# Kernel optimization log

Hardware: AMD Instinct MI355X
Metric: run time of the kernel (lower is better)

The kernel has to match this reference:

```python
import jax, jax.numpy as jnp
import numpy as np

EPS_LN = 1e-6
EPS_NORM = 1e-7


def conv1x1(x, w, b):
    # x: [B,Cin,H,W], w: [Cout,Cin], b: [Cout]
    return jnp.einsum('bchw,oc->bohw', x, w) + b[None, :, None, None]


def ln2d(x, g, beta):
    u = x.mean(1, keepdims=True)
    s = ((x - u) ** 2).mean(1, keepdims=True)
    return g[None, :, None, None] * ((x - u) / jnp.sqrt(s + EPS_LN)) + beta[None, :, None, None]


def gather_neighborhoods(x, r):
    # x: [B,C,H,W] -> [B,C,n,H,W] with zero padding, n=(2r+1)**2
    B, C, H, W = x.shape
    xp = jnp.pad(x, ((0, 0), (0, 0), (r, r), (r, r)))
    slices = [xp[:, :, dy:dy + H, dx:dx + W]
              for dy in range(2 * r + 1) for dx in range(2 * r + 1)]
    return jnp.stack(slices, axis=2)


def valid_mask(H, W, r):
    offs = jnp.arange(-r, r + 1)
    hh = jnp.arange(H)
    ww = jnp.arange(W)
    vy = ((hh[None, :] + offs[:, None]) >= 0) & ((hh[None, :] + offs[:, None]) < H)  # [d,H]
    vx = ((ww[None, :] + offs[:, None]) >= 0) & ((ww[None, :] + offs[:, None]) < W)  # [d,W]
    return (vy[:, None, :, None] & vx[None, :, None, :]).reshape((2 * r + 1) ** 2, H, W)


def setup_inputs() -> dict:
    key = jax.random.key(0)
    B, C, H, W, r = 2, 64, 112, 112, 3
    n2 = (2 * r + 1) ** 2  # 49
    ks = jax.random.split(key, 16)
    s = 0.02
    inp = {
        'spatial_feats': jax.random.normal(ks[0], (B, C, H, W), jnp.float32),
        'semantic_feats': jax.random.normal(ks[1], (B, C, H, W), jnp.float32),
        # range_proj: conv1x1 -> LN2d -> SiLU -> conv1x1
        'rp_w1': s * jax.random.normal(ks[2], (C, C), jnp.float32), 'rp_b1': jnp.zeros((C,), jnp.float32),
        'rp_g': jnp.ones((C,), jnp.float32), 'rp_beta': jnp.zeros((C,), jnp.float32),
        'rp_w2': s * jax.random.normal(ks[3], (C, C), jnp.float32), 'rp_b2': jnp.zeros((C,), jnp.float32),
        # fixup_proj: conv1x1 (n2+C -> n2) -> LN2d -> SiLU -> conv1x1 (n2->n2)
        'fx_w1': s * jax.random.normal(ks[4], (n2, n2 + C), jnp.float32), 'fx_b1': jnp.zeros((n2,), jnp.float32),
        'fx_g': jnp.ones((n2,), jnp.float32), 'fx_beta': jnp.zeros((n2,), jnp.float32),
        'fx_w2': s * jax.random.normal(ks[5], (n2, n2), jnp.float32), 'fx_b2': jnp.zeros((n2,), jnp.float32),
        # output_proj: conv1x1 -> LN2d -> conv1x1
        'op_w1': s * jax.random.normal(ks[6], (C, C), jnp.float32), 'op_b1': jnp.zeros((C,), jnp.float32),
        'op_g': jnp.ones((C,), jnp.float32), 'op_beta': jnp.zeros((C,), jnp.float32),
        'op_w2': s * jax.random.normal(ks[7], (C, C), jnp.float32), 'op_b2': jnp.zeros((C,), jnp.float32),
        'sigma_spatial': jnp.array(1.0, jnp.float32),
    }
    return inp


def reference(spatial_feats, semantic_feats,
              rp_w1, rp_b1, rp_g, rp_beta, rp_w2, rp_b2,
              fx_w1, fx_b1, fx_g, fx_beta, fx_w2, fx_b2,
              op_w1, op_b1, op_g, op_beta, op_w2, op_b2,
              sigma_spatial):
    r = 3
    B, C, H, W = spatial_feats.shape
    # range_proj(semantic)
    px = conv1x1(semantic_feats, rp_w1, rp_b1)
    px = jax.nn.silu(ln2d(px, rp_g, rp_beta))
    px = conv1x1(px, rp_w2, rp_b2)

    # bilateral combined kernel: spatial Gaussian * range Gaussian, zero outside bounds
    offs = jnp.arange(-r, r + 1, dtype=jnp.float32)
    d2 = (offs[:, None] ** 2 + offs[None, :] ** 2).reshape(-1)  # [n2]
    sw = jnp.exp(-d2 / (2.0 * sigma_spatial ** 2))              # [n2]

    nbr = gather_neighborhoods(px, r)                            # [B,C,n2,H,W]
    nbr_sq = (nbr ** 2).sum(1)                                   # [B,n2,H,W]
    ctr_sq = (px ** 2).sum(1)                                    # [B,H,W]
    dot = jnp.einsum('bcnhw,bchw->bnhw', nbr, px)
    dist2 = jnp.maximum(nbr_sq + ctr_sq[:, None] - 2.0 * dot, 0.0)
    rw = jnp.exp(-dist2 / (2.0 * C))                             # range Gaussian, scale^2 = dim

    valid = valid_mask(H, W, r).astype(px.dtype)                 # [n2,H,W]
    combined = rw * sw[None, :, None, None] * valid[None]        # [B,n2,H,W]

    # gated fixup
    f = conv1x1(jnp.concatenate([combined, semantic_feats], axis=1), fx_w1, fx_b1)
    f = jax.nn.silu(ln2d(f, fx_g, fx_beta))
    f = conv1x1(f, fx_w2, fx_b2)
    combined = combined * (1.0 + jax.nn.sigmoid(f))
    combined = combined / (combined.sum(1, keepdims=True) + EPS_NORM)

    # neighborhood-weighted reduction of spatial feats
    nbhd = gather_neighborhoods(spatial_feats, r)                # [B,C,n2,H,W]
    out = jnp.einsum('bcnhw,bnhw->bchw', nbhd, combined)

    out = conv1x1(out, op_w1, op_b1)
    out = ln2d(out, op_g, op_beta)
    out = conv1x1(out, op_w2, op_b2)
    return out
```

## Files before the change

kernel.cpp:

```cpp
#include <hip/hip_runtime.h>

typedef unsigned short ushort;
typedef unsigned int uint;

constexpr int B = 2, C = 64, H = 112, W = 112;
constexpr int HW = H * W;
constexpr int NPIX = B * HW;
constexpr int NBLK = 512;
constexpr float EPS_LN = 1e-6f, EPS_NORM = 1e-7f;

typedef __attribute__((ext_vector_type(8))) short bf16x8;
typedef __attribute__((ext_vector_type(4))) float f32x4;

__device__ __forceinline__ float rcp_fast(float x) { return __builtin_amdgcn_rcpf(x); }
__device__ __forceinline__ float sigmoid_f(float x) { return rcp_fast(1.f + __expf(-x)); }
__device__ __forceinline__ int uni(int x) { return __builtin_amdgcn_readfirstlane(x); }
__device__ __forceinline__ int div7s(int x)  { return (x * 9363) >> 16; }
__device__ __forceinline__ int div13s(int x) { return (x * 5042) >> 16; }
__device__ __forceinline__ int div49s(int x) { return (x * 1338) >> 16; }

__device__ __forceinline__ ushort rne16(float x) {
    uint u = __float_as_uint(x);
    u += 0x7fffu + ((u >> 16) & 1u);
    return (ushort)(u >> 16);
}
__device__ __forceinline__ uint pack2(float a, float b) {
    return (uint)rne16(a) | ((uint)rne16(b) << 16);
}
__device__ __forceinline__ float2 up2(uint u) {
    return make_float2(__uint_as_float(u << 16), __uint_as_float(u & 0xffff0000u));
}

__device__ __forceinline__ f32x4 mfma16(bf16x8 a, bf16x8 b, f32x4 c) {
    return __builtin_amdgcn_mfma_f32_16x16x32_bf16(a, b, c, 0, 0, 0);
}

__device__ __forceinline__ void decode_blk(int blk, int& b, int& ty, int& tx) {
    int p8 = blk & 7, i = blk >> 3;
    b = p8 >> 2;
    int quad = p8 & 3;
    int lty = i >> 3, ltx = i & 7;
    ty = (quad >> 1) * 8 + lty;
    tx = (quad & 1) * 8 + ltx;
}

__device__ __forceinline__ void stage_w(const float* __restrict__ wsrc,
                                        ushort* wh, ushort* wl, int tid)
{
#pragma unroll
    for (int i = 0; i < 8; ++i) {
        int idx2 = i * 256 + tid;
        int o = idx2 >> 5, k = (idx2 & 31) * 2;
        float2 xy = *(const float2*)&wsrc[o * 64 + k];
        uint h = pack2(xy.x, xy.y);
        *(uint*)&wh[o * 72 + k] = h;
        *(uint*)&wl[o * 72 + k] = pack2(xy.x - __uint_as_float((h & 0xffffu) << 16),
                                        xy.y - __uint_as_float(h & 0xffff0000u));
    }
}

__device__ __forceinline__ void gemm64(const ushort* __restrict__ wh, const ushort* __restrict__ wl,
                                       const ushort* __restrict__ xh, const ushort* __restrict__ xl,
                                       const float* __restrict__ bias,
                                       int lm, int l4, int pp, f32x4 acc[4])
{
#pragma unroll
    for (int mt = 0; mt < 4; ++mt) {
        const int ob = mt * 16 + l4 * 4;
        acc[mt][0] = bias[ob]; acc[mt][1] = bias[ob + 1];
        acc[mt][2] = bias[ob + 2]; acc[mt][3] = bias[ob + 3];
    }
#pragma unroll
    for (int kt = 0; kt < 2; ++kt) {
        const int xo = pp * 72 + kt * 32 + l4 * 8;
        bf16x8 bh = *(const bf16x8*)&xh[xo];
        bf16x8 bl = *(const bf16x8*)&xl[xo];
#pragma unroll
        for (int mt = 0; mt < 4; ++mt) {
            const int wo = (mt * 16 + lm) * 72 + kt * 32 + l4 * 8;
            bf16x8 ah = *(const bf16x8*)&wh[wo];
            bf16x8 al = *(const bf16x8*)&wl[wo];
            acc[mt] = mfma16(al, bh, acc[mt]);
            acc[mt] = mfma16(ah, bl, acc[mt]);
            acc[mt] = mfma16(ah, bh, acc[mt]);
        }
    }
}

__global__ __launch_bounds__(256) void k1_range_proj(
    const float* __restrict__ sem,
    const float* __restrict__ w1, const float* __restrict__ b1,
    const float* __restrict__ g,  const float* __restrict__ be,
    const float* __restrict__ w2, const float* __restrict__ b2,
    ushort* __restrict__ px16, float* __restrict__ sqnorm)
{
    __shared__ __align__(16) ushort u16[28160];
    ushort* wh1 = u16;
    ushort* wl1 = u16 + 4608;
    ushort* wh2 = u16 + 9216;
    ushort* wl2 = u16 + 13824;
    ushort* xh  = u16 + 18432;
    ushort* xl  = u16 + 23040;
    float*  bv  = (float*)(u16 + 27648);

    const int tid = threadIdx.x, lane = tid & 63, wv = tid >> 6;
    const int lm = lane & 15, l4 = lane >> 4;
    int b, ty, tx; decode_blk(blockIdx.x, b, ty, tx);

    {
        const int lp = lane < 49 ? lane : 48;
        const int py = div7s(lp), px = lp - py * 7;
        const int hw = (ty * 7 + py) * W + tx * 7 + px;
        const bool a = lane < 49;
        float xv[16];
#pragma unroll
        for (int j = 0; j < 16; ++j)
            xv[j] = a ? sem[(size_t)(b * 64 + wv * 16 + j) * HW + hw] : 0.f;
        uint hu[8], lu[8];
#pragma unroll
        for (int jj = 0; jj < 8; ++jj) {
            uint hh = pack2(xv[2 * jj], xv[2 * jj + 1]);
            hu[jj] = hh;
            lu[jj] = pack2(xv[2 * jj]     - __uint_as_float((hh & 0xffffu) << 16),
                           xv[2 * jj + 1] - __uint_as_float(hh & 0xffff0000u));
        }
        const int rb = lane * 72 + wv * 16;
        *(uint4*)&xh[rb]     = make_uint4(hu[0], hu[1], hu[2], hu[3]);
        *(uint4*)&xh[rb + 8] = make_uint4(hu[4], hu[5], hu[6], hu[7]);
        *(uint4*)&xl[rb]     = make_uint4(lu[0], lu[1], lu[2], lu[3]);
        *(uint4*)&xl[rb + 8] = make_uint4(lu[4], lu[5], lu[6], lu[7]);
    }
    stage_w(w1, wh1, wl1, tid);
    stage_w(w2, wh2, wl2, tid);
    if (tid < 64) { bv[tid] = b1[tid]; bv[64 + tid] = g[tid];
                    bv[128 + tid] = be[tid]; bv[192 + tid] = b2[tid]; }
    __syncthreads();

    const int pp = wv * 16 + lm;
    f32x4 f[4];
    gemm64(wh1, wl1, xh, xl, bv, lm, l4, pp, f);

    float psum = 0.f, psq = 0.f;
#pragma unroll
    for (int mt = 0; mt < 4; ++mt)
#pragma unroll
        for (int r = 0; r < 4; ++r) { float fv = f[mt][r]; psum += fv; psq += fv * fv; }
    psum += __shfl_xor(psum, 16); psum += __shfl_xor(psum, 32);
    psq  += __shfl_xor(psq, 16);  psq  += __shfl_xor(psq, 32);
    const float m = psum * (1.f / 64.f);
    const float rstd = rsqrtf(psq * (1.f / 64.f) - m * m + EPS_LN);

    float sv_[16];
#pragma unroll
    for (int mt = 0; mt < 4; ++mt)
#pragma unroll
        for (int r = 0; r < 4; ++r) {
            const int o = mt * 16 + l4 * 4 + r;
            float y = bv[64 + o] * (f[mt][r] - m) * rstd + bv[128 + o];
            sv_[mt * 4 + r] = y * sigmoid_f(y);
        }
    __syncthreads();
#pragma unroll
    for (int mt = 0; mt < 4; ++mt) {
        uint h0 = pack2(sv_[4 * mt],     sv_[4 * mt + 1]);
        uint h1 = pack2(sv_[4 * mt + 2], sv_[4 * mt + 3]);
        uint l0 = pack2(sv_[4 * mt]     - __uint_as_float((h0 & 0xffffu) << 16),
                        sv_[4 * mt + 1] - __uint_as_float(h0 & 0xffff0000u));
        uint l1 = pack2(sv_[4 * mt + 2] - __uint_as_float((h1 & 0xffffu) << 16),
                        sv_[4 * mt + 3] - __uint_as_float(h1 & 0xffff0000u));
        const int so = pp * 72 + mt * 16 + l4 * 4;
        *(uint2*)&xh[so] = make_uint2(h0, h1);
        *(uint2*)&xl[so] = make_uint2(l0, l1);
    }
    __syncthreads();

    f32x4 z[4];
    gemm64(wh2, wl2, xh, xl, bv + 192, lm, l4, pp, z);

    float sq = 0.f;
#pragma unroll
    for (int mt = 0; mt < 4; ++mt)
#pragma unroll
        for (int r = 0; r < 4; ++r) sq += z[mt][r] * z[mt][r];
    sq += __shfl_xor(sq, 16); sq += __shfl_xor(sq, 32);

    if (pp < 49) {
        const int py = div7s(pp), px = pp - py * 7;
        const int hwi = (ty * 7 + py) * W + tx * 7 + px;
        ushort* dst = &px16[((size_t)b * HW + hwi) * 64];
#pragma unroll
        for (int mt = 0; mt < 4; ++mt)
            *(uint2*)&dst[mt * 16 + l4 * 4] =
                make_uint2(pack2(z[mt][0], z[mt][1]), pack2(z[mt][2], z[mt][3]));
        if (l4 == 0) sqnorm[(size_t)b * HW + hwi] = sq;
    }
}

__global__ __launch_bounds__(256, 2) void k23_fused(
    const ushort* __restrict__ px16, const float* __restrict__ sqnorm,
    const float* __restrict__ sem,  const float* __restrict__ spat,
    const float* __restrict__ fw1, const float* __restrict__ fb1,
    const float* __restrict__ fg,  const float* __restrict__ fbe,
    const float* __restrict__ fw2, const float* __restrict__ fb2,
    const float* __restrict__ w1, const float* __restrict__ b1,
    const float* __restrict__ g,  const float* __restrict__ be,
    const float* __restrict__ w2, const float* __restrict__ b2,
    const float* __restrict__ sigma_, float* __restrict__ out)
{
    __shared__ __align__(16) float smem[18048];
    ushort* haloA = (ushort*)smem;
    ushort* haloB = (ushort*)(smem + 5408);
    float*  comb  = smem + 10816;
    float*  fscr  = smem + 13952;
    float*  sqn_l = smem + 17088;
    float*  pm3   = smem + 17264;
    float*  ps3   = smem + 17520;
    float*  pt    = smem + 17776;
    float*  fwc  = smem;
    float*  fw2l = smem + 2401;
    ushort* whiP = (ushort*)smem;
    ushort* wloP = (ushort*)smem + 4608;
    ushort* ahiP = (ushort*)(smem + 5408);
    ushort* aloP = (ushort*)(smem + 5408) + 4608;
    float*  bvP  = smem + 13952;

    const int tid = threadIdx.x, lane = tid & 63, wv = tid >> 6;
    const int lm = lane & 15, l4 = lane >> 6 == 0 ? (lane >> 4) : 0;
    int b, ty, tx; decode_blk(blockIdx.x, b, ty, tx);
    const int lp  = lane < 49 ? lane : 48;
    const int py  = div7s(lp), pxl = lp - py * 7;
    const int h = ty * 7 + py, w = tx * 7 + pxl;
    const int hw = h * W + w;
    const int h0 = ty * 7 - 3, w0 = tx * 7 - 3;
    const bool act = lane < 49;

    float sv[64];
#pragma unroll
    for (int k = 0; k < 64; ++k) sv[k] = sem[(size_t)(b * 64 + k) * HW + hw];

    if (tid < 169) {
        const int ry = div13s(tid), rx = tid - ry * 13;
        const int hh = h0 + ry, ww = w0 + rx;
        const bool valid = (unsigned)hh < (unsigned)H && (unsigned)ww < (unsigned)W;
        const int soff = hh * W + ww;
        const int rsw = (tid & 7), rb_ = tid << 6;
#pragma unroll
        for (int cq = 0; cq < 8; ++cq) {
            uint4 v = make_uint4(0u, 0u, 0u, 0u);
            if (valid) {
                const float* sp = &spat[(size_t)(b * 64 + 8 * cq) * HW + soff];
                v.x = pack2(sp[0],      sp[HW]);
                v.y = pack2(sp[2 * HW], sp[3 * HW]);
                v.z = pack2(sp[4 * HW], sp[5 * HW]);
                v.w = pack2(sp[6 * HW], sp[7 * HW]);
            }
            *(uint4*)&haloB[rb_ + ((cq ^ rsw) << 3)] = v;
        }
    }

    for (int i = 0; i < 6; ++i) {
        int idx = i * 256 + tid;
        if (idx < 1352) {
            int r = idx >> 3, q = idx & 7;
            int ry = div13s(r), rx = r - ry * 13;
            int hh = h0 + ry, ww = w0 + rx;
            bool valid = (unsigned)hh < (unsigned)H && (unsigned)ww < (unsigned)W;
            uint4 v = make_uint4(0u, 0u, 0u, 0u);
            if (valid) v = *(const uint4*)&px16[((size_t)b * HW + hh * W + ww) * 64 + 8 * q];
            *(uint4*)&haloA[(r << 6) + ((q ^ (r & 7)) << 3)] = v;
        }
    }
    if (tid < 169) {
        int ry = div13s(tid), rx = tid - ry * 13;
        int hh = h0 + ry, ww = w0 + rx;
        bool valid = (unsigned)hh < (unsigned)H && (unsigned)ww < (unsigned)W;
        float v = 0.f;
        if (valid) v = sqnorm[(size_t)b * HW + hh * W + ww];
        sqn_l[tid] = v;
    }
    __syncthreads();

    const int rbase = py * 13 + pxl;
    const int rp = rbase + 42;
    {
        float cv[64];
#pragma unroll
        for (int q = 0; q < 8; ++q) {
            uint4 v = *(const uint4*)&haloA[(rp << 6) + ((q ^ (rp & 7)) << 3)];
            float2 p0_ = up2(v.x), p1_ = up2(v.y), p2_ = up2(v.z), p3_ = up2(v.w);
            cv[8 * q + 0] = p0_.x; cv[8 * q + 1] = p0_.y;
            cv[8 * q + 2] = p1_.x; cv[8 * q + 3] = p1_.y;
            cv[8 * q + 4] = p2_.x; cv[8 * q + 5] = p2_.y;
            cv[8 * q + 6] = p3_.x; cv[8 * q + 7] = p3_.y;
        }
        const float sqc = sqn_l[rp];
        const float sg_ = sigma_[0];
        const float inv2s2 = rcp_fast(2.f * sg_ * sg_);
        for (int i = 0; i < 13; ++i) {
            int n = uni(wv + 4 * i);
            if (n < 49) {
                int ryn = div7s(n), rxn = n - ryn * 7;
                int dy = ryn - 3, dx = rxn - 3;
                int rn = rbase + ryn * 13 + rxn;
                float d0 = 0, d1 = 0, d2 = 0, d3 = 0;
#pragma unroll
                for (int q = 0; q < 8; ++q) {
                    uint4 v = *(const uint4*)&haloA[(rn << 6) + ((q ^ (rn & 7)) << 3)];
                    float2 a = up2(v.x), bb = up2(v.y), c = up2(v.z), d = up2(v.w);
                    d0 += a.x  * cv[8 * q + 0]; d1 += a.y  * cv[8 * q + 1];
                    d2 += bb.x * cv[8 * q + 2]; d3 += bb.y * cv[8 * q + 3];
                    d0 += c.x  * cv[8 * q + 4]; d1 += c.y  * cv[8 * q + 5];
                    d2 += d.x  * cv[8 * q + 6]; d3 += d.y  * cv[8 * q + 7];
                }
                float dot = (d0 + d1) + (d2 + d3);
                float dist2 = fmaxf(sqn_l[rn] + sqc - 2.f * dot, 0.f);
                bool validn = (unsigned)(h + dy) < (unsigned)H && (unsigned)(w + dx) < (unsigned)W;
                float d2n = (float)(dy * dy + dx * dx);
                comb[n * 64 + lane] = validn ? __expf(-(dist2 * (1.f / 128.f) + d2n * inv2s2)) : 0.f;
            }
        }
    }
    __syncthreads();

    for (int i = tid; i < 2401; i += 256) {
        int o = div49s(i);
        fwc[i]  = fw1[o * 113 + (i - o * 49)];
        fw2l[i] = fw2[i];
    }
    __syncthreads();

    float cb[49];
#pragma unroll
    for (int n = 0; n < 49; ++n) cb[n] = comb[n * 64 + lane];
    float macc = 0.f, sacc = 0.f;
    for (int i = 0; i < 13; ++i) {
        const int o = uni(wv + 4 * i);
        if (o < 49) {
            const float* wr = &fwc[o * 49];
            float a0 = 0, a1 = 0, a2 = 0, a3 = 0;
#pragma unroll
            for (int k = 0; k < 48; k += 4) {
                a0 += wr[k] * cb[k];       a1 += wr[k + 1] * cb[k + 1];
                a2 += wr[k + 2] * cb[k + 2]; a3 += wr[k + 3] * cb[k + 3];
            }
            a0 += wr[48] * cb[48];
            const float* wr2 = &fw1[o * 113 + 49];
#pragma unroll
            for (int k = 0; k < 64; k += 4) {
                a0 += wr2[k] * sv[k];       a1 += wr2[k + 1] * sv[k + 1];
                a2 += wr2[k + 2] * sv[k + 2]; a3 += wr2[k + 3] * sv[k + 3];
            }
            float f = (a0 + a1) + (a2 + a3) + fb1[o];
            fscr[o * 64 + lane] = f;
            macc += f; sacc += f * f;
        }
    }
    pm3[wv * 64 + lane] = macc; ps3[wv * 64 + lane] = sacc;
    __syncthreads();
    {
        float m  = (pm3[lane] + pm3[64 + lane] + pm3[128 + lane] + pm3[192 + lane]) * (1.f / 49.f);
        float va = (ps3[lane] + ps3[64 + lane] + ps3[128 + lane] + ps3[192 + lane]) * (1.f / 49.f) - m * m;
        float rstd = rsqrtf(va + EPS_LN);
        float s[49];
#pragma unroll
        for (int k = 0; k < 49; ++k) {
            float y = fg[k] * (fscr[k * 64 + lane] - m) * rstd + fbe[k];
            s[k] = y * sigmoid_f(y);
        }
        float tacc = 0.f;
        for (int i = 0; i < 13; ++i) {
            const int o = uni(wv + 4 * i);
            if (o < 49) {
                const float* wr = &fw2l[o * 49];
                float a0 = 0, a1 = 0, a2 = 0, a3 = 0;
#pragma unroll
                for (int k = 0; k < 48; k += 4) {
                    a0 += wr[k] * s[k];       a1 += wr[k + 1] * s[k + 1];
                    a2 += wr[k + 2] * s[k + 2]; a3 += wr[k + 3] * s[k + 3];
                }
                a0 += wr[48] * s[48];
                float fo = (a0 + a1) + (a2 + a3) + fb2[o];
                float gate = 1.f + sigmoid_f(fo);
                float cx = comb[o * 64 + lane] * gate;
                comb[o * 64 + lane] = cx;
                tacc += cx;
            }
        }
        pt[wv * 64 + lane] = tacc;
    }
    __syncthreads();
    const float inv = rcp_fast(pt[lane] + pt[64 + lane] + pt[128 + lane] + pt[192 + lane] + EPS_NORM);

    stage_w(w1, whiP, wloP, tid);
    if (tid < 64) { bvP[tid] = b1[tid]; bvP[64 + tid] = g[tid];
                    bvP[128 + tid] = be[tid]; bvP[192 + tid] = b2[tid]; }

    const int c0 = uni(wv * 16);
    const int qq0 = c0 >> 3;
    float acc[16];
#pragma unroll
    for (int j = 0; j < 16; ++j) acc[j] = 0.f;
    for (int n = 0; n < 49; ++n) {
        int ryn = n / 7, rxn = n - ryn * 7;
        int rn = rbase + ryn * 13 + rxn;
        float cn = comb[n * 64 + lane] * inv;
        const int rb_ = rn << 6, rsw = rn & 7;
#pragma unroll
        for (int q = 0; q < 2; ++q) {
            uint4 v = *(const uint4*)&haloB[rb_ + (((qq0 + q) ^ rsw) << 3)];
            float2 a = up2(v.x), bb = up2(v.y), c = up2(v.z), d = up2(v.w);
            acc[8 * q + 0] += cn * a.x;  acc[8 * q + 1] += cn * a.y;
            acc[8 * q + 2] += cn * bb.x; acc[8 * q + 3] += cn * bb.y;
            acc[8 * q + 4] += cn * c.x;  acc[8 * q + 5] += cn * c.y;
            acc[8 * q + 6] += cn * d.x;  acc[8 * q + 7] += cn * d.y;
        }
    }
    __syncthreads();

    {
        uint hu[8], lu[8];
#pragma unroll
        for (int jj = 0; jj < 8; ++jj) {
            float x0 = act ? acc[2 * jj] : 0.f;
            float x1 = act ? acc[2 * jj + 1] : 0.f;
            uint hh = pack2(x0, x1);
            hu[jj] = hh;
            lu[jj] = pack2(x0 - __uint_as_float((hh & 0xffffu) << 16),
                           x1 - __uint_as_float(hh & 0xffff0000u));
        }
        const int rb = lane * 72 + c0;
        *(uint4*)&ahiP[rb]     = make_uint4(hu[0], hu[1], hu[2], hu[3]);
        *(uint4*)&ahiP[rb + 8] = make_uint4(hu[4], hu[5], hu[6], hu[7]);
        *(uint4*)&aloP[rb]     = make_uint4(lu[0], lu[1], lu[2], lu[3]);
        *(uint4*)&aloP[rb + 8] = make_uint4(lu[4], lu[5], lu[6], lu[7]);
    }
    __syncthreads();

    const int pp = wv * 16 + lm;
    f32x4 f6[4];
    gemm64(whiP, wloP, ahiP, aloP, bvP, lm, l4, pp, f6);

    float psum = 0.f, psq = 0.f;
#pragma unroll
    for (int mt = 0; mt < 4; ++mt)
#pragma unroll
        for (int r = 0; r < 4; ++r) { float fv = f6[mt][r]; psum += fv; psq += fv * fv; }
    psum += __shfl_xor(psum, 16); psum += __shfl_xor(psum, 32);
    psq  += __shfl_xor(psq, 16);  psq  += __shfl_xor(psq, 32);
    const float m6 = psum * (1.f / 64.f);
    const float rstd6 = rsqrtf(psq * (1.f / 64.f) - m6 * m6 + EPS_LN);

    float yv[16];
#pragma unroll
    for (int mt = 0; mt < 4; ++mt)
#pragma unroll
        for (int r = 0; r < 4; ++r) {
            const int o = mt * 16 + l4 * 4 + r;
            yv[mt * 4 + r] = bvP[64 + o] * (f6[mt][r] - m6) * rstd6 + bvP[128 + o];
        }
    __syncthreads();

#pragma unroll
    for (int mt = 0; mt < 4; ++mt) {
        uint h0 = pack2(yv[4 * mt],     yv[4 * mt + 1]);
        uint h1 = pack2(yv[4 * mt + 2], yv[4 * mt + 3]);
        uint l0 = pack2(yv[4 * mt]     - __uint_as_float((h0 & 0xffffu) << 16),
                        yv[4 * mt + 1] - __uint_as_float(h0 & 0xffff0000u));
        uint l1 = pack2(yv[4 * mt + 2] - __uint_as_float((h1 & 0xffffu) << 16),
                        yv[4 * mt + 3] - __uint_as_float(h1 & 0xffff0000u));
        const int so = pp * 72 + mt * 16 + l4 * 4;
        *(uint2*)&ahiP[so] = make_uint2(h0, h1);
        *(uint2*)&aloP[so] = make_uint2(l0, l1);
    }
    stage_w(w2, whiP, wloP, tid);
    __syncthreads();

    f32x4 z6[4];
    gemm64(whiP, wloP, ahiP, aloP, bvP + 192, lm, l4, pp, z6);

    if (pp < 49) {
        const int py6 = div7s(pp), px6 = pp - py6 * 7;
        const int hwi6 = (ty * 7 + py6) * W + tx * 7 + px6;
#pragma unroll
        for (int mt = 0; mt < 4; ++mt)
#pragma unroll
            for (int r = 0; r < 4; ++r)
                out[(size_t)(b * 64 + mt * 16 + l4 * 4 + r) * HW + hwi6] = z6[mt][r];
    }
}

extern "C" void kernel_launch(void* const* d_in, const int* in_sizes, int n_in,
                              void* d_out, int out_size, void* d_ws, size_t ws_size,
                              hipStream_t stream)
{
    const float* spatial  = (const float*)d_in[0];
    const float* semantic = (const float*)d_in[1];
    const float* rp_w1 = (const float*)d_in[2];
    const float* rp_b1 = (const float*)d_in[3];
    const float* rp_g  = (const float*)d_in[4];
    const float* rp_be = (const float*)d_in[5];
    const float* rp_w2 = (const float*)d_in[6];
    const float* rp_b2 = (const float*)d_in[7];
    const float* fx_w1 = (const float*)d_in[8];
    const float* fx_b1 = (const float*)d_in[9];
    const float* fx_g  = (const float*)d_in[10];
    const float* fx_be = (const float*)d_in[11];
    const float* fx_w2 = (const float*)d_in[12];
    const float* fx_b2 = (const float*)d_in[13];
    const float* op_w1 = (const float*)d_in[14];
    const float* op_b1 = (const float*)d_in[15];
    const float* op_g  = (const float*)d_in[16];
    const float* op_be = (const float*)d_in[17];
    const float* op_w2 = (const float*)d_in[18];
    const float* op_b2 = (const float*)d_in[19];
    const float* sigma = (const float*)d_in[20];

    ushort* px16  = (ushort*)d_ws;
    float* sqnorm = (float*)((char*)d_ws + (size_t)NPIX * 64 * 2);

    k1_range_proj<<<NBLK, 256, 0, stream>>>(
        semantic, rp_w1, rp_b1, rp_g, rp_be, rp_w2, rp_b2, px16, sqnorm);
    k23_fused<<<NBLK, 256, 0, stream>>>(
        px16, sqnorm, semantic, spatial,
        fx_w1, fx_b1, fx_g, fx_be, fx_w2, fx_b2,
        op_w1, op_b1, op_g, op_be, op_w2, op_b2,
        sigma, (float*)d_out);
}
```

Baseline: 159.0 us.

## Compute neighborhood dot products with MFMA over the halo tile

Replaces the per-lane scalar bf16 dot-product loop (64 channels × 49 neighbors per pixel) with MFMA 16x16 matmuls. These compute the full halo-rows × center-pixels dot matrix into shared memory, and the range weights are then read from that matrix. The spatial halo load (haloB) moves after the range-weight stage, which means the dot matrix can reuse that region, and the fixup weight load is merged into the same barrier phase. This trades redundant scalar FMAs for a larger shared-memory matrix of 176 rows, which includes rows no pixel ever needs, plus an extra barrier and store/load round trip.

```diff
diff --git a/kernel.cpp b/kernel.cpp
--- a/kernel.cpp
+++ b/kernel.cpp
@@ -216,6 +216,7 @@
     float*  pm3   = smem + 17264;
     float*  ps3   = smem + 17520;
     float*  pt    = smem + 17776;
+    float*  dmat  = smem + 5408;
     float*  fwc  = smem;
     float*  fw2l = smem + 2401;
     ushort* whiP = (ushort*)smem;
@@ -225,7 +226,7 @@
     float*  bvP  = smem + 13952;
 
     const int tid = threadIdx.x, lane = tid & 63, wv = tid >> 6;
-    const int lm = lane & 15, l4 = lane >> 6 == 0 ? (lane >> 4) : 0;
+    const int lm = lane & 15, l4 = lane >> 4;
     int b, ty, tx; decode_blk(blockIdx.x, b, ty, tx);
     const int lp  = lane < 49 ? lane : 48;
     const int py  = div7s(lp), pxl = lp - py * 7;
@@ -238,6 +239,86 @@
 #pragma unroll
     for (int k = 0; k < 64; ++k) sv[k] = sem[(size_t)(b * 64 + k) * HW + hw];
 
+    for (int i = 0; i < 6; ++i) {
+        int idx = i * 256 + tid;
+        if (idx < 1352) {
+            int r = idx >> 3, q = idx & 7;
+            int ry = div13s(r), rx = r - ry * 13;
+            int hh = h0 + ry, ww = w0 + rx;
+            bool valid = (unsigned)hh < (unsigned)H && (unsigned)ww < (unsigned)W;
+            uint4 v = make_uint4(0u, 0u, 0u, 0u);
+            if (valid) v = *(const uint4*)&px16[((size_t)b * HW + hh * W + ww) * 64 + 8 * q];
+            *(uint4*)&haloA[(r << 6) + ((q ^ (r & 7)) << 3)] = v;
+        }
+    }
+    if (tid < 169) {
+        int ry = div13s(tid), rx = tid - ry * 13;
+        int hh = h0 + ry, ww = w0 + rx;
+        bool valid = (unsigned)hh < (unsigned)H && (unsigned)ww < (unsigned)W;
+        float v = 0.f;
+        if (valid) v = sqnorm[(size_t)b * HW + hh * W + ww];
+        sqn_l[tid] = v;
+    }
+    __syncthreads();
+
+    {
+        const int pp2 = wv * 16 + lm;
+        const int qp = pp2 < 49 ? pp2 : 48;
+        const int pyp = div7s(qp), pxp = qp - pyp * 7;
+        const int rpp = pyp * 13 + pxp + 42;
+        bf16x8 bc0 = *(const bf16x8*)&haloA[(rpp << 6) + ((l4 ^ (rpp & 7)) << 3)];
+        bf16x8 bc1 = *(const bf16x8*)&haloA[(rpp << 6) + (((4 + l4) ^ (rpp & 7)) << 3)];
+#pragma unroll
+        for (int mt = 0; mt < 11; ++mt) {
+            const int r = mt * 16 + lm;
+            bf16x8 a0 = *(const bf16x8*)&haloA[(r << 6) + ((l4 ^ (r & 7)) << 3)];
+            bf16x8 a1 = *(const bf16x8*)&haloA[(r << 6) + (((4 + l4) ^ (r & 7)) << 3)];
+            f32x4 d = {0.f, 0.f, 0.f, 0.f};
+            d = mfma16(a0, bc0, d);
+            d = mfma16(a1, bc1, d);
+            const int orow = mt * 16 + l4 * 4;
+#pragma unroll
+            for (int rr = 0; rr < 4; ++rr)
+                dmat[(orow + rr) * 66 + pp2] = d[rr];
+        }
+    }
+    __syncthreads();
+
+    const int rbase = py * 13 + pxl;
+    const int rp = rbase + 42;
+    float cbl[13];
+    {
+        const float sqc = sqn_l[rp];
+        const float sg_ = sigma_[0];
+        const float inv2s2 = rcp_fast(2.f * sg_ * sg_);
+#pragma unroll
+        for (int i = 0; i < 13; ++i) {
+            const int n = uni(wv + 4 * i);
+            cbl[i] = 0.f;
+            if (n < 49) {
+                int ryn = div7s(n), rxn = n - ryn * 7;
+                int dy = ryn - 3, dx = rxn - 3;
+                int rn = rbase + ryn * 13 + rxn;
+                float dot = dmat[rn * 66 + lane];
+                float dist2 = fmaxf(sqn_l[rn] + sqc - 2.f * dot, 0.f);
+                bool validn = (unsigned)(h + dy) < (unsigned)H && (unsigned)(w + dx) < (unsigned)W;
+                float d2n = (float)(dy * dy + dx * dx);
+                cbl[i] = validn ? __expf(-(dist2 * (1.f / 128.f) + d2n * inv2s2)) : 0.f;
+            }
+        }
+    }
+    for (int i = tid; i < 2401; i += 256) {
+        int o = div49s(i);
+        fwc[i]  = fw1[o * 113 + (i - o * 49)];
+        fw2l[i] = fw2[i];
+    }
+    __syncthreads();
+
+#pragma unroll
+    for (int i = 0; i < 13; ++i) {
+        const int n = wv + 4 * i;
+        if (n < 49) comb[n * 64 + lane] = cbl[i];
+    }
     if (tid < 169) {
         const int ry = div13s(tid), rx = tid - ry * 13;
         const int hh = h0 + ry, ww = w0 + rx;
@@ -256,76 +337,6 @@
             }
             *(uint4*)&haloB[rb_ + ((cq ^ rsw) << 3)] = v;
         }
-    }
-
-    for (int i = 0; i < 6; ++i) {
-        int idx = i * 256 + tid;
-        if (idx < 1352) {
-            int r = idx >> 3, q = idx & 7;
-            int ry = div13s(r), rx = r - ry * 13;
-            int hh = h0 + ry, ww = w0 + rx;
-            bool valid = (unsigned)hh < (unsigned)H && (unsigned)ww < (unsigned)W;
-            uint4 v = make_uint4(0u, 0u, 0u, 0u);
-            if (valid) v = *(const uint4*)&px16[((size_t)b * HW + hh * W + ww) * 64 + 8 * q];
-            *(uint4*)&haloA[(r << 6) + ((q ^ (r & 7)) << 3)] = v;
-        }
-    }
-    if (tid < 169) {
-        int ry = div13s(tid), rx = tid - ry * 13;
-        int hh = h0 + ry, ww = w0 + rx;
-        bool valid = (unsigned)hh < (unsigned)H && (unsigned)ww < (unsigned)W;
-        float v = 0.f;
-        if (valid) v = sqnorm[(size_t)b * HW + hh * W + ww];
-        sqn_l[tid] = v;
-    }
-    __syncthreads();
-
-    const int rbase = py * 13 + pxl;
-    const int rp = rbase + 42;
-    {
-        float cv[64];
-#pragma unroll
-        for (int q = 0; q < 8; ++q) {
-            uint4 v = *(const uint4*)&haloA[(rp << 6) + ((q ^ (rp & 7)) << 3)];
-            float2 p0_ = up2(v.x), p1_ = up2(v.y), p2_ = up2(v.z), p3_ = up2(v.w);
-            cv[8 * q + 0] = p0_.x; cv[8 * q + 1] = p0_.y;
-            cv[8 * q + 2] = p1_.x; cv[8 * q + 3] = p1_.y;
-            cv[8 * q + 4] = p2_.x; cv[8 * q + 5] = p2_.y;
-            cv[8 * q + 6] = p3_.x; cv[8 * q + 7] = p3_.y;
-        }
-        const float sqc = sqn_l[rp];
-        const float sg_ = sigma_[0];
-        const float inv2s2 = rcp_fast(2.f * sg_ * sg_);
-        for (int i = 0; i < 13; ++i) {
-            int n = uni(wv + 4 * i);
-            if (n < 49) {
-                int ryn = div7s(n), rxn = n - ryn * 7;
-                int dy = ryn - 3, dx = rxn - 3;
-                int rn = rbase + ryn * 13 + rxn;
-                float d0 = 0, d1 = 0, d2 = 0, d3 = 0;
-#pragma unroll
-                for (int q = 0; q < 8; ++q) {
-                    uint4 v = *(const uint4*)&haloA[(rn << 6) + ((q ^ (rn & 7)) << 3)];
-                    float2 a = up2(v.x), bb = up2(v.y), c = up2(v.z), d = up2(v.w);
-                    d0 += a.x  * cv[8 * q + 0]; d1 += a.y  * cv[8 * q + 1];
-                    d2 += bb.x * cv[8 * q + 2]; d3 += bb.y * cv[8 * q + 3];
-                    d0 += c.x  * cv[8 * q + 4]; d1 += c.y  * cv[8 * q + 5];
-                    d2 += d.x  * cv[8 * q + 6]; d3 += d.y  * cv[8 * q + 7];
-                }
-                float dot = (d0 + d1) + (d2 + d3);
-                float dist2 = fmaxf(sqn_l[rn] + sqc - 2.f * dot, 0.f);
-                bool validn = (unsigned)(h + dy) < (unsigned)H && (unsigned)(w + dx) < (unsigned)W;
-                float d2n = (float)(dy * dy + dx * dx);
-                comb[n * 64 + lane] = validn ? __expf(-(dist2 * (1.f / 128.f) + d2n * inv2s2)) : 0.f;
-            }
-        }
-    }
-    __syncthreads();
-
-    for (int i = tid; i < 2401; i += 256) {
-        int o = div49s(i);
-        fwc[i]  = fw1[o * 113 + (i - o * 49)];
-        fw2l[i] = fw2[i];
     }
     __syncthreads();
 
```

Measured after the change: 155.8 us. 2.0% less time.
